# Kernel optimization log

Measured on AMD Instinct MI355X. Metric: run time of the kernel, lower is better.

## Reference

```python
import jax, jax.numpy as jnp
import numpy as np

NUM_HEADS = 8


def setup_inputs() -> dict:
    key = jax.random.key(0)
    ks = jax.random.split(key, 7)
    B, H, W, C = 1, 64, 64, 512
    x = jax.random.normal(ks[0], (B, H, W, C), dtype=jnp.float32)
    # lat in [-pi/2, pi/2), lon in [0, 2*pi) radians
    lat_grid = (jax.random.uniform(ks[1], (H, W), dtype=jnp.float32) - 0.5) * np.float32(np.pi)
    lon_grid = jax.random.uniform(ks[2], (H, W), dtype=jnp.float32) * np.float32(2 * np.pi)
    w_qkv = jax.random.normal(ks[3], (3 * C, C), dtype=jnp.float32) * 0.02
    b_qkv = jax.random.normal(ks[4], (3 * C,), dtype=jnp.float32) * 0.02
    w_out = jax.random.normal(ks[5], (C, C), dtype=jnp.float32) * 0.02
    b_out = jax.random.normal(ks[6], (C,), dtype=jnp.float32) * 0.02
    return {"x": x, "lat_grid": lat_grid, "lon_grid": lon_grid,
            "w_qkv": w_qkv, "b_qkv": b_qkv, "w_out": w_out, "b_out": b_out}


def _distance_bias(lat_grid, lon_grid):
    # Haversine great-circle distance between all pairs of grid points.
    lat = lat_grid.reshape(-1)  # [N]
    lon = lon_grid.reshape(-1)
    dlat = lat[None, :] - lat[:, None]  # [N, N]
    dlon = lon[None, :] - lon[:, None]
    a = jnp.sin(dlat / 2) ** 2 + jnp.cos(lat)[:, None] * jnp.cos(lat)[None, :] * jnp.sin(dlon / 2) ** 2
    dist = 2.0 * jnp.arcsin(jnp.sqrt(jnp.clip(a, 0.0, 1.0)))
    # torch .std() is unbiased (ddof=1)
    return -dist / jnp.std(dist, ddof=1)


def reference(x, lat_grid, lon_grid, w_qkv, b_qkv, w_out, b_out):
    B, H, W, C = x.shape
    nh = NUM_HEADS
    dh = C // nh
    N = H * W
    qkv = x @ w_qkv.T + b_qkv  # [B, H, W, 3C]
    qkv = qkv.reshape(B, N, 3, nh, dh)
    q = jnp.transpose(qkv[:, :, 0], (0, 2, 1, 3))  # [B, nh, N, dh]
    k = jnp.transpose(qkv[:, :, 1], (0, 2, 1, 3))
    v = jnp.transpose(qkv[:, :, 2], (0, 2, 1, 3))
    scale = np.float32(1.0 / np.sqrt(dh))
    attn = jnp.einsum("bhnd,bhmd->bhnm", q, k) * scale  # [B, nh, N, N]
    attn = attn + _distance_bias(lat_grid, lon_grid)[None, None]
    attn = jax.nn.softmax(attn, axis=-1)  # dropout is identity in eval
    out = jnp.einsum("bhnm,bhmd->bhnd", attn, v)  # [B, nh, N, dh]
    out = jnp.transpose(out, (0, 2, 1, 3)).reshape(B, H, W, C)
    return out @ w_out.T + b_out
```

## Files before the change

kernel.cpp:

```cpp
#include <hip/hip_runtime.h>
#include <hip/hip_bf16.h>


typedef __attribute__((ext_vector_type(8))) short bf16x8;
typedef __attribute__((ext_vector_type(4))) float f32x4;

#define MFMA16(a, b, c) __builtin_amdgcn_mfma_f32_16x16x32_bf16(a, b, c, 0, 0, 0)

__device__ __forceinline__ unsigned short f2b(float f) {
    union { float f; unsigned int i; } v;
    v.f = f;
    unsigned int lsb = (v.i >> 16) & 1u;
    unsigned int r = v.i + 0x7fffu + lsb;
    return (unsigned short)(r >> 16);
}

__global__ __launch_bounds__(256) void cvt_frag(
    const float* __restrict__ in, unsigned short* __restrict__ out) {
    int t = blockIdx.x * 256 + threadIdx.x;
    int l = t & 15, qd = (t >> 4) & 3, c = (t >> 6) & 15, g = t >> 10;
    const float* src = in + ((size_t)g * 16 + l) * 512 + c * 32 + qd * 8;
    float4 v0 = *(const float4*)src;
    float4 v1 = *(const float4*)(src + 4);
    ushort4 u0, u1;
    u0.x = f2b(v0.x); u0.y = f2b(v0.y); u0.z = f2b(v0.z); u0.w = f2b(v0.w);
    u1.x = f2b(v1.x); u1.y = f2b(v1.y); u1.z = f2b(v1.z); u1.w = f2b(v1.w);
    unsigned short* dst = out + (size_t)t * 8;
    *(ushort4*)dst = u0;
    *(ushort4*)(dst + 4) = u1;
}

__global__ __launch_bounds__(256) void dist_kernel(
    const float* __restrict__ lat, const float* __restrict__ lon,
    float* __restrict__ dist, double* __restrict__ partials) {
    __shared__ float sl_i[64], sc_i[64], so_i[64];
    __shared__ float sl_j[64], sc_j[64], so_j[64];
    __shared__ double rs[256], rs2[256];

    int bi = blockIdx.x;
    int i0 = (bi >> 6) << 6;
    int j0 = (bi & 63) << 6;
    int tid = threadIdx.x;

    if (tid < 64) {
        float la = lat[i0 + tid];
        sl_i[tid] = la; sc_i[tid] = __cosf(la); so_i[tid] = lon[i0 + tid];
    } else if (tid < 128) {
        int t = tid - 64;
        float la = lat[j0 + t];
        sl_j[t] = la; sc_j[t] = __cosf(la); so_j[t] = lon[j0 + t];
    }
    __syncthreads();

    double s = 0.0, s2 = 0.0;
    int col = tid & 63;
    int pcol = ((col & 15) << 2) + (col >> 4);
    float latj = sl_j[col], cj = sc_j[col], lonj = so_j[col];
#pragma unroll
    for (int kk = 0; kk < 16; kk++) {
        int row = (kk << 2) + (tid >> 6);
        float dlat = latj - sl_i[row];
        float dlon = lonj - so_i[row];
        float h1 = __sinf(0.5f * dlat);
        float h2 = __sinf(0.5f * dlon);
        float a = h1 * h1 + sc_i[row] * cj * h2 * h2;
        a = fminf(fmaxf(a, 0.0f), 1.0f);
        float d = 2.0f * asinf(sqrtf(a));
        dist[(size_t)(i0 + row) * 4096 + j0 + pcol] = d;
        s += (double)d;
        s2 += (double)d * (double)d;
    }
    rs[tid] = s; rs2[tid] = s2;
    __syncthreads();
    for (int off = 128; off > 0; off >>= 1) {
        if (tid < off) { rs[tid] += rs[tid + off]; rs2[tid] += rs2[tid + off]; }
        __syncthreads();
    }
    if (tid == 0) {
        partials[2 * bi] = rs[0];
        partials[2 * bi + 1] = rs2[0];
    }
}

__global__ __launch_bounds__(256) void stats_kernel(
    const double* __restrict__ partials, float* __restrict__ neg_inv_std) {
    __shared__ double rs[256], rs2[256];
    int tid = threadIdx.x;
    double s = 0.0, s2 = 0.0;
    for (int i = tid; i < 4096; i += 256) {
        s += partials[2 * i];
        s2 += partials[2 * i + 1];
    }
    rs[tid] = s; rs2[tid] = s2;
    __syncthreads();
    for (int off = 128; off > 0; off >>= 1) {
        if (tid < off) { rs[tid] += rs[tid + off]; rs2[tid] += rs2[tid + off]; }
        __syncthreads();
    }
    if (tid == 0) {
        double n = 16777216.0;
        double mean = rs[0] / n;
        double var = (rs2[0] - n * mean * mean) / (n - 1.0);
        *neg_inv_std = (float)(-1.0 / sqrt(var));
    }
}

__global__ __launch_bounds__(256) void qkv_gemm(
    const unsigned short* __restrict__ x, const unsigned short* __restrict__ w,
    const float* __restrict__ b,
    unsigned short* __restrict__ q, unsigned short* __restrict__ k,
    unsigned short* __restrict__ vt) {
    __shared__ unsigned short stage[64][72];
    int lane = threadIdx.x & 63, wave = threadIdx.x >> 6;
    int l16 = lane & 15, quad = lane >> 4;
    int m0 = blockIdx.y * 64 + wave * 16;
    int n0 = blockIdx.x * 64;

    const unsigned short* abase = x + (size_t)(blockIdx.y * 4 + wave) * 8192 + lane * 8;
    f32x4 acc[4];
#pragma unroll
    for (int nb = 0; nb < 4; nb++) acc[nb] = (f32x4){0.f, 0.f, 0.f, 0.f};

    for (int k0 = 0; k0 < 512; k0 += 32) {
        bf16x8 af = *(const bf16x8*)(abase + (k0 >> 5) * 512);
#pragma unroll
        for (int nb = 0; nb < 4; nb++) {
            bf16x8 bf = *(const bf16x8*)(w + (size_t)((n0 >> 4) + nb) * 8192
                                           + (k0 >> 5) * 512 + lane * 8);
            acc[nb] = MFMA16(af, bf, acc[nb]);
        }
    }
    if (blockIdx.x < 8) {
#pragma unroll
        for (int nb = 0; nb < 4; nb++) {
            int j = n0 + nb * 16 + l16;
            float bj = b[j];
            int h = j >> 6, d = j & 63;
#pragma unroll
            for (int r = 0; r < 4; r++) {
                int n = m0 + quad * 4 + r;
                q[((size_t)h * 4096 + n) * 64 + d] = f2b((acc[nb][r] + bj) * 0.125f);
            }
        }
    } else if (blockIdx.x < 16) {
        int h = blockIdx.x - 8;
#pragma unroll
        for (int nb = 0; nb < 4; nb++) {
            int d = nb * 16 + l16;
            float bj = b[512 + h * 64 + d];
#pragma unroll
            for (int r = 0; r < 4; r++)
                stage[wave * 16 + quad * 4 + r][d] = f2b(acc[nb][r] + bj);
        }
        __syncthreads();
        unsigned short* kb = k + ((size_t)h << 18) + (size_t)blockIdx.y * 4096;
#pragma unroll
        for (int p = 0; p < 2; p++) {
            int rid = p * 256 + threadIdx.x;
            int t = rid >> 7;
            int rem = rid & 127;
            int half = rem >> 6, qd = (rem >> 4) & 3, l = rem & 15;
            const unsigned short* src = &stage[t * 16 + l][half * 32 + qd * 8];
            unsigned short* dst = kb + t * 1024 + half * 512 + qd * 128 + l * 8;
            *(uint4*)dst = *(const uint4*)src;
        }
    } else {
        int h = blockIdx.x - 16;
#pragma unroll
        for (int nb = 0; nb < 4; nb++) {
            int d = nb * 16 + l16;
            float bj = b[1024 + h * 64 + d];
#pragma unroll
            for (int r = 0; r < 4; r++)
                stage[d][quad * 16 + r * 4 + wave] = f2b(acc[nb][r] + bj);
        }
        __syncthreads();
        int t = threadIdx.x;
        int d = t >> 2;
        int nq = (t & 3) * 16;
        unsigned short* dst = vt + ((size_t)h << 18) + (size_t)blockIdx.y * 4096
                            + (d >> 4) * 1024 + ((nq >> 5) & 1) * 512
                            + ((nq >> 3) & 3) * 128 + (d & 15) * 8;
        const unsigned short* src = &stage[d][nq];
        *(uint4*)dst = *(const uint4*)src;
        *(uint4*)(dst + 128) = *(const uint4*)(src + 8);
    }
}

__device__ __forceinline__ void attn_step(
    const unsigned short* __restrict__ kptr, const unsigned short* __restrict__ vtp,
    short* __restrict__ pb, int h, int kv0, int lane, int l16, int quad,
    bf16x8 qf0, bf16x8 qf1, float4 (&dv)[4], const float* __restrict__ drow,
    int kv_next, float nis, f32x4 (&o)[4], float (&lam)[4]) {
    size_t tbase = ((size_t)h << 18) + ((size_t)kv0 << 6) + lane * 8;
    const unsigned short* kb = kptr + tbase;
    const unsigned short* vb = vtp + tbase;
    f32x4 s[4];
#pragma unroll
    for (int cb = 0; cb < 4; cb++) {
        bf16x8 kf0 = *(const bf16x8*)(kb + cb * 1024);
        bf16x8 kf1 = *(const bf16x8*)(kb + cb * 1024 + 512);
        f32x4 z = (f32x4){0.f, 0.f, 0.f, 0.f};
        z = MFMA16(qf0, kf0, z);
        z = MFMA16(qf1, kf1, z);
        s[cb] = z;
    }
#pragma unroll
    for (int r = 0; r < 4; r++) {
        s[0][r] = fmaf(dv[r].x, nis, s[0][r]);
        s[1][r] = fmaf(dv[r].y, nis, s[1][r]);
        s[2][r] = fmaf(dv[r].z, nis, s[2][r]);
        s[3][r] = fmaf(dv[r].w, nis, s[3][r]);
    }
#pragma unroll
    for (int r = 0; r < 4; r++)
        dv[r] = *(const float4*)(drow + (size_t)r * 4096 + kv_next);
#pragma unroll
    for (int r = 0; r < 4; r++) {
        float p0 = __expf(s[0][r]);
        float p1 = __expf(s[1][r]);
        float p2 = __expf(s[2][r]);
        float p3 = __expf(s[3][r]);
        lam[r] += (p0 + p1) + (p2 + p3);
        unsigned int w0 = (unsigned int)f2b(p0) | ((unsigned int)f2b(p1) << 16);
        unsigned int w1 = (unsigned int)f2b(p2) | ((unsigned int)f2b(p3) << 16);
        uint2 pk; pk.x = w0; pk.y = w1;
        *(uint2*)(pb + (quad * 4 + r) * 72 + l16 * 4) = pk;
    }
    bf16x8 pf0 = *(const bf16x8*)(pb + l16 * 72 + quad * 8);
    bf16x8 pf1 = *(const bf16x8*)(pb + l16 * 72 + 32 + quad * 8);
#pragma unroll
    for (int db = 0; db < 4; db++) {
        bf16x8 vf0 = *(const bf16x8*)(vb + db * 1024);
        bf16x8 vf1 = *(const bf16x8*)(vb + db * 1024 + 512);
        o[db] = MFMA16(pf0, vf0, o[db]);
        o[db] = MFMA16(pf1, vf1, o[db]);
    }
}

__global__ __launch_bounds__(1024, 4) void attn_kernel(
    const unsigned short* __restrict__ q, const unsigned short* __restrict__ k,
    const unsigned short* __restrict__ vt, const float* __restrict__ dist,
    const float* __restrict__ nis_p, unsigned short* __restrict__ att) {
    __shared__ __align__(16) char smem[36864];
    int tid = threadIdx.x;
    int lane = tid & 63, wave = tid >> 6;
    int l16 = lane & 15, quad = lane >> 4;
    int b = blockIdx.x;
    int xcd = b & 7, j = b >> 3;
    int h  = (xcd & 3) * 2 + (j & 1);
    int qs = (xcd >> 2) * 32 + (j >> 1);
    int qgl = wave & 3;
    int qt = wave >> 2;
    int q0 = qs * 64 + qgl * 16;
    int kvbase = qt * 1024;
    float nis = *nis_p;

    short* pb = (short*)smem + wave * 1152;

    const unsigned short* qbase = q + ((size_t)h * 4096 + q0 + l16) * 64 + quad * 8;
    bf16x8 qf0 = *(const bf16x8*)(qbase);
    bf16x8 qf1 = *(const bf16x8*)(qbase + 32);

    f32x4 o[4];
    float lam[4];
#pragma unroll
    for (int r = 0; r < 4; r++) {
        lam[r] = 0.f;
        o[0][r] = 0.f; o[1][r] = 0.f; o[2][r] = 0.f; o[3][r] = 0.f;
    }

    const float* drow = dist + (size_t)(q0 + quad * 4) * 4096 + l16 * 4;
    float4 dv[4];
#pragma unroll
    for (int r = 0; r < 4; r++)
        dv[r] = *(const float4*)(drow + (size_t)r * 4096 + kvbase);

    for (int it = 0; it < 16; ++it) {
        int kv0 = kvbase + it * 64;
        int kvn = (it == 15) ? kvbase : kv0 + 64;
        attn_step(k, vt, pb, h, kv0, lane, l16, quad, qf0, qf1, dv, drow, kvn,
                  nis, o, lam);
    }

#pragma unroll
    for (int r = 0; r < 4; r++)
#pragma unroll
        for (int off = 1; off < 16; off <<= 1)
            lam[r] += __shfl_xor(lam[r], off, 64);

    __syncthreads();
    float* obuf = (float*)smem;
    float* lbuf = (float*)(smem + 16384);
    if (l16 == 0)
#pragma unroll
        for (int r = 0; r < 4; r++)
            lbuf[qt * 64 + qgl * 16 + quad * 4 + r] = lam[r];
    if (qt == 0) {
#pragma unroll
        for (int db = 0; db < 4; db++)
#pragma unroll
            for (int r = 0; r < 4; r++)
                obuf[(qgl * 16 + quad * 4 + r) * 64 + db * 16 + l16] = o[db][r];
    }
    __syncthreads();
    if (qt == 1) {
#pragma unroll
        for (int db = 0; db < 4; db++)
#pragma unroll
            for (int r = 0; r < 4; r++)
                obuf[(qgl * 16 + quad * 4 + r) * 64 + db * 16 + l16] += o[db][r];
    }
    __syncthreads();
    if (qt == 2) {
#pragma unroll
        for (int db = 0; db < 4; db++)
#pragma unroll
            for (int r = 0; r < 4; r++)
                obuf[(qgl * 16 + quad * 4 + r) * 64 + db * 16 + l16] += o[db][r];
    }
    __syncthreads();
    if (qt == 3) {
#pragma unroll
        for (int db = 0; db < 4; db++)
#pragma unroll
            for (int r = 0; r < 4; r++)
                obuf[(qgl * 16 + quad * 4 + r) * 64 + db * 16 + l16] += o[db][r];
    }
    __syncthreads();

    int rl = tid >> 4;
    int d4 = (tid & 15) * 4;
    float L = lbuf[rl] + lbuf[64 + rl] + lbuf[128 + rl] + lbuf[192 + rl];
    float rinv = 1.0f / L;
    const float* ob = obuf + rl * 64 + d4;
    ushort4 ua;
    ua.x = f2b(ob[0] * rinv); ua.y = f2b(ob[1] * rinv);
    ua.z = f2b(ob[2] * rinv); ua.w = f2b(ob[3] * rinv);
    int row = qs * 64 + rl;
    int col = h * 64 + d4;
    size_t dst = (size_t)(row >> 4) * 8192 + (col >> 5) * 512
               + ((col >> 3) & 3) * 128 + (row & 15) * 8 + (col & 7);
    *(ushort4*)(att + dst) = ua;
}

__global__ __launch_bounds__(256) void out_gemm(
    const unsigned short* __restrict__ att, const unsigned short* __restrict__ w,
    const float* __restrict__ b, float* __restrict__ out) {
    int lane = threadIdx.x & 63, wave = threadIdx.x >> 6;
    int l16 = lane & 15, quad = lane >> 4;
    int m0 = blockIdx.y * 64 + wave * 16;
    int n0 = blockIdx.x * 64;

    const unsigned short* abase = att + (size_t)(blockIdx.y * 4 + wave) * 8192 + lane * 8;
    f32x4 acc[4];
#pragma unroll
    for (int nb = 0; nb < 4; nb++) acc[nb] = (f32x4){0.f, 0.f, 0.f, 0.f};

    for (int k0 = 0; k0 < 512; k0 += 32) {
        bf16x8 af = *(const bf16x8*)(abase + (k0 >> 5) * 512);
#pragma unroll
        for (int nb = 0; nb < 4; nb++) {
            bf16x8 bf = *(const bf16x8*)(w + (size_t)((n0 >> 4) + nb) * 8192
                                           + (k0 >> 5) * 512 + lane * 8);
            acc[nb] = MFMA16(af, bf, acc[nb]);
        }
    }
#pragma unroll
    for (int nb = 0; nb < 4; nb++) {
        float bj = b[n0 + nb * 16 + l16];
#pragma unroll
        for (int r = 0; r < 4; r++)
            out[(size_t)(m0 + quad * 4 + r) * 512 + n0 + nb * 16 + l16] =
                acc[nb][r] + bj;
    }
}

extern "C" void kernel_launch(void* const* d_in, const int* in_sizes, int n_in,
                              void* d_out, int out_size, void* d_ws, size_t ws_size,
                              hipStream_t stream) {
    const float* x    = (const float*)d_in[0];
    const float* lat  = (const float*)d_in[1];
    const float* lon  = (const float*)d_in[2];
    const float* wqkv = (const float*)d_in[3];
    const float* bqkv = (const float*)d_in[4];
    const float* wout = (const float*)d_in[5];
    const float* bout = (const float*)d_in[6];
    float* out = (float*)d_out;

    char* ws = (char*)d_ws;
    float* dist        = (float*)ws;
    double* partials   = (double*)(ws + 67108864);
    float* nis         = (float*)(ws + 67108864 + 65536);
    unsigned short* q  = (unsigned short*)(ws + 67108864 + 65600);
    unsigned short* k  = q  + (size_t)8 * 4096 * 64;
    unsigned short* vt = k  + (size_t)8 * 4096 * 64;
    unsigned short* att = vt + (size_t)8 * 4096 * 64;
    unsigned short* xb  = att + (size_t)4096 * 512;
    unsigned short* wqb = xb  + (size_t)4096 * 512;
    unsigned short* wob = wqb + (size_t)1536 * 512;

    cvt_frag<<<1024, 256, 0, stream>>>(x, xb);
    cvt_frag<<<384, 256, 0, stream>>>(wqkv, wqb);
    cvt_frag<<<128, 256, 0, stream>>>(wout, wob);
    dist_kernel<<<4096, 256, 0, stream>>>(lat, lon, dist, partials);
    stats_kernel<<<1, 256, 0, stream>>>(partials, nis);
    qkv_gemm<<<dim3(24, 64), 256, 0, stream>>>(xb, wqb, bqkv, q, k, vt);
    attn_kernel<<<512, 1024, 0, stream>>>(q, k, vt, dist, nis, att);
    out_gemm<<<dim3(8, 64), 256, 0, stream>>>(att, wob, bout, out);
}
```

Measured before the change: 231.4 us.

## Fuse prep kernels into one launch and halve attention block size

Merges the three fp32-to-bf16 fragment conversions and the haversine distance kernel into a single prep_kernel launch, dispatching on block index. The per-thread distance partial sums now accumulate in float instead of double. Attention blocks shrink from 1024 to 512 threads, each covering 32 query rows instead of 64, with twice as many blocks and half the shared memory. The goal is lower launch overhead and finer-grained attention work for better CU fill, at the cost of less K/V reuse per block and slightly lower precision in the statistics.

New measurement: 223.2 us. 1.04x faster.

```diff
diff --git a/kernel.cpp b/kernel.cpp
--- a/kernel.cpp
+++ b/kernel.cpp
@@ -15,9 +15,68 @@
     return (unsigned short)(r >> 16);
 }
 
-__global__ __launch_bounds__(256) void cvt_frag(
-    const float* __restrict__ in, unsigned short* __restrict__ out) {
-    int t = blockIdx.x * 256 + threadIdx.x;
+__global__ __launch_bounds__(256) void prep_kernel(
+    const float* __restrict__ lat, const float* __restrict__ lon,
+    float* __restrict__ dist, double* __restrict__ partials,
+    const float* __restrict__ x, unsigned short* __restrict__ xb,
+    const float* __restrict__ wq, unsigned short* __restrict__ wqb,
+    const float* __restrict__ wo, unsigned short* __restrict__ wob) {
+    __shared__ float sl_i[64], sc_i[64], so_i[64];
+    __shared__ float sl_j[64], sc_j[64], so_j[64];
+    __shared__ double rs[256], rs2[256];
+
+    int b = blockIdx.x;
+    int tid = threadIdx.x;
+
+    if (b < 4096) {
+        int i0 = (b >> 6) << 6;
+        int j0 = (b & 63) << 6;
+
+        if (tid < 64) {
+            float la = lat[i0 + tid];
+            sl_i[tid] = la; sc_i[tid] = __cosf(la); so_i[tid] = lon[i0 + tid];
+        } else if (tid < 128) {
+            int t = tid - 64;
+            float la = lat[j0 + t];
+            sl_j[t] = la; sc_j[t] = __cosf(la); so_j[t] = lon[j0 + t];
+        }
+        __syncthreads();
+
+        float s = 0.f, s2 = 0.f;
+        int col = tid & 63;
+        int pcol = ((col & 15) << 2) + (col >> 4);
+        float latj = sl_j[col], cj = sc_j[col], lonj = so_j[col];
+#pragma unroll
+        for (int kk = 0; kk < 16; kk++) {
+            int row = (kk << 2) + (tid >> 6);
+            float dlat = latj - sl_i[row];
+            float dlon = lonj - so_i[row];
+            float h1 = __sinf(0.5f * dlat);
+            float h2 = __sinf(0.5f * dlon);
+            float a = h1 * h1 + sc_i[row] * cj * h2 * h2;
+            a = fminf(fmaxf(a, 0.0f), 1.0f);
+            float d = 2.0f * asinf(sqrtf(a));
+            dist[(size_t)(i0 + row) * 4096 + j0 + pcol] = d;
+            s += d;
+            s2 += d * d;
+        }
+        rs[tid] = (double)s; rs2[tid] = (double)s2;
+        __syncthreads();
+        for (int off = 128; off > 0; off >>= 1) {
+            if (tid < off) { rs[tid] += rs[tid + off]; rs2[tid] += rs2[tid + off]; }
+            __syncthreads();
+        }
+        if (tid == 0) {
+            partials[2 * b] = rs[0];
+            partials[2 * b + 1] = rs2[0];
+        }
+        return;
+    }
+
+    const float* in; unsigned short* out; int t;
+    if (b < 5120)      { in = x;  out = xb;  t = (b - 4096) * 256 + tid; }
+    else if (b < 5504) { in = wq; out = wqb; t = (b - 5120) * 256 + tid; }
+    else               { in = wo; out = wob; t = (b - 5504) * 256 + tid; }
     int l = t & 15, qd = (t >> 4) & 3, c = (t >> 6) & 15, g = t >> 10;
     const float* src = in + ((size_t)g * 16 + l) * 512 + c * 32 + qd * 8;
     float4 v0 = *(const float4*)src;
@@ -30,58 +89,6 @@
     *(ushort4*)(dst + 4) = u1;
 }
 
-__global__ __launch_bounds__(256) void dist_kernel(
-    const float* __restrict__ lat, const float* __restrict__ lon,
-    float* __restrict__ dist, double* __restrict__ partials) {
-    __shared__ float sl_i[64], sc_i[64], so_i[64];
-    __shared__ float sl_j[64], sc_j[64], so_j[64];
-    __shared__ double rs[256], rs2[256];
-
-    int bi = blockIdx.x;
-    int i0 = (bi >> 6) << 6;
-    int j0 = (bi & 63) << 6;
-    int tid = threadIdx.x;
-
-    if (tid < 64) {
-        float la = lat[i0 + tid];
-        sl_i[tid] = la; sc_i[tid] = __cosf(la); so_i[tid] = lon[i0 + tid];
-    } else if (tid < 128) {
-        int t = tid - 64;
-        float la = lat[j0 + t];
-        sl_j[t] = la; sc_j[t] = __cosf(la); so_j[t] = lon[j0 + t];
-    }
-    __syncthreads();
-
-    double s = 0.0, s2 = 0.0;
-    int col = tid & 63;
-    int pcol = ((col & 15) << 2) + (col >> 4);
-    float latj = sl_j[col], cj = sc_j[col], lonj = so_j[col];
-#pragma unroll
-    for (int kk = 0; kk < 16; kk++) {
-        int row = (kk << 2) + (tid >> 6);
-        float dlat = latj - sl_i[row];
-        float dlon = lonj - so_i[row];
-        float h1 = __sinf(0.5f * dlat);
-        float h2 = __sinf(0.5f * dlon);
-        float a = h1 * h1 + sc_i[row] * cj * h2 * h2;
-        a = fminf(fmaxf(a, 0.0f), 1.0f);
-        float d = 2.0f * asinf(sqrtf(a));
-        dist[(size_t)(i0 + row) * 4096 + j0 + pcol] = d;
-        s += (double)d;
-        s2 += (double)d * (double)d;
-    }
-    rs[tid] = s; rs2[tid] = s2;
-    __syncthreads();
-    for (int off = 128; off > 0; off >>= 1) {
-        if (tid < off) { rs[tid] += rs[tid + off]; rs2[tid] += rs2[tid + off]; }
-        __syncthreads();
-    }
-    if (tid == 0) {
-        partials[2 * bi] = rs[0];
-        partials[2 * bi + 1] = rs2[0];
-    }
-}
-
 __global__ __launch_bounds__(256) void stats_kernel(
     const double* __restrict__ partials, float* __restrict__ neg_inv_std) {
     __shared__ double rs[256], rs2[256];
@@ -238,21 +245,21 @@
     }
 }
 
-__global__ __launch_bounds__(1024, 4) void attn_kernel(
+__global__ __launch_bounds__(512, 4) void attn_kernel(
     const unsigned short* __restrict__ q, const unsigned short* __restrict__ k,
     const unsigned short* __restrict__ vt, const float* __restrict__ dist,
     const float* __restrict__ nis_p, unsigned short* __restrict__ att) {
-    __shared__ __align__(16) char smem[36864];
+    __shared__ __align__(16) char smem[18432];
     int tid = threadIdx.x;
     int lane = tid & 63, wave = tid >> 6;
     int l16 = lane & 15, quad = lane >> 4;
     int b = blockIdx.x;
     int xcd = b & 7, j = b >> 3;
     int h  = (xcd & 3) * 2 + (j & 1);
-    int qs = (xcd >> 2) * 32 + (j >> 1);
-    int qgl = wave & 3;
-    int qt = wave >> 2;
-    int q0 = qs * 64 + qgl * 16;
+    int qs = (xcd >> 2) * 64 + (j >> 1);
+    int qgl = wave & 1;
+    int qt = wave >> 1;
+    int q0 = qs * 32 + qgl * 16;
     int kvbase = qt * 1024;
     float nis = *nis_p;
 
@@ -291,11 +298,11 @@
 
     __syncthreads();
     float* obuf = (float*)smem;
-    float* lbuf = (float*)(smem + 16384);
+    float* lbuf = (float*)(smem + 8192);
     if (l16 == 0)
 #pragma unroll
         for (int r = 0; r < 4; r++)
-            lbuf[qt * 64 + qgl * 16 + quad * 4 + r] = lam[r];
+            lbuf[qt * 32 + qgl * 16 + quad * 4 + r] = lam[r];
     if (qt == 0) {
 #pragma unroll
         for (int db = 0; db < 4; db++)
@@ -331,13 +338,13 @@
 
     int rl = tid >> 4;
     int d4 = (tid & 15) * 4;
-    float L = lbuf[rl] + lbuf[64 + rl] + lbuf[128 + rl] + lbuf[192 + rl];
+    float L = lbuf[rl] + lbuf[32 + rl] + lbuf[64 + rl] + lbuf[96 + rl];
     float rinv = 1.0f / L;
     const float* ob = obuf + rl * 64 + d4;
     ushort4 ua;
     ua.x = f2b(ob[0] * rinv); ua.y = f2b(ob[1] * rinv);
     ua.z = f2b(ob[2] * rinv); ua.w = f2b(ob[3] * rinv);
-    int row = qs * 64 + rl;
+    int row = qs * 32 + rl;
     int col = h * 64 + d4;
     size_t dst = (size_t)(row >> 4) * 8192 + (col >> 5) * 512
                + ((col >> 3) & 3) * 128 + (row & 15) * 8 + (col & 7);
@@ -400,12 +407,10 @@
     unsigned short* wqb = xb  + (size_t)4096 * 512;
     unsigned short* wob = wqb + (size_t)1536 * 512;
 
-    cvt_frag<<<1024, 256, 0, stream>>>(x, xb);
-    cvt_frag<<<384, 256, 0, stream>>>(wqkv, wqb);
-    cvt_frag<<<128, 256, 0, stream>>>(wout, wob);
-    dist_kernel<<<4096, 256, 0, stream>>>(lat, lon, dist, partials);
+    prep_kernel<<<5632, 256, 0, stream>>>(lat, lon, dist, partials,
+                                          x, xb, wqkv, wqb, wout, wob);
     stats_kernel<<<1, 256, 0, stream>>>(partials, nis);
     qkv_gemm<<<dim3(24, 64), 256, 0, stream>>>(xb, wqb, bqkv, q, k, vt);
-    attn_kernel<<<512, 1024, 0, stream>>>(q, k, vt, dist, nis, att);
+    attn_kernel<<<1024, 512, 0, stream>>>(q, k, vt, dist, nis, att);
     out_gemm<<<dim3(8, 64), 256, 0, stream>>>(att, wob, bout, out);
 }
```
